# Kernel optimization log

Measured on AMD Instinct MI355X. Metric: run time of the kernel, lower is better.

## Reference

```python
import jax, jax.numpy as jnp
import numpy as np

WINDOW = 8
NUM_HEADS = 12


def setup_inputs() -> dict:
    key = jax.random.key(0)
    k1, k2, k3 = jax.random.split(key, 3)
    B, H, W, C = 32, 64, 64, 384
    x = jax.random.normal(k1, (B, H, W, C), dtype=jnp.float32)
    w_qkv = jax.random.normal(k2, (C, 3 * C), dtype=jnp.float32) * (C ** -0.5)
    w_proj = jax.random.normal(k3, (C, C), dtype=jnp.float32) * (C ** -0.5)
    b_proj = jnp.zeros((C,), dtype=jnp.float32)
    return {"x": x, "w_qkv": w_qkv, "w_proj": w_proj, "b_proj": b_proj}


def window_partition(x, ws):
    B, H, W, C = x.shape
    x = x.reshape(B, H // ws, ws, W // ws, ws, C)
    x = x.transpose(0, 1, 3, 2, 4, 5)  # [B, nH, nW, ws, ws, C]
    return x.reshape(-1, ws * ws, C)


def window_reverse(x, ws, H, W):
    nWin = (H // ws) * (W // ws)
    B = x.shape[0] // nWin
    C = x.shape[2]
    x = x.reshape(B, H // ws, W // ws, ws, ws, C)
    x = x.transpose(0, 1, 3, 2, 4, 5)
    return x.reshape(B, H, W, C)


def reference(x, w_qkv, w_proj, b_proj):
    B, H, W, C = x.shape
    ws = WINDOW
    nh = NUM_HEADS
    hd = C // nh
    scale = hd ** -0.5
    N = ws * ws

    xw = window_partition(x, ws)                      # [nW*B, N, C]
    qkv = xw @ w_qkv                                  # [nW*B, N, 3C]
    qkv = qkv.reshape(-1, N, 3, nh, hd)
    qkv = qkv.transpose(2, 0, 3, 1, 4)                # [3, nW*B, nh, N, hd]
    q, k, v = qkv[0], qkv[1], qkv[2]

    attn = jnp.einsum('whnd,whmd->whnm', q, k) * scale  # [nW*B, nh, N, N]
    attn = jax.nn.softmax(attn, axis=-1)
    out = jnp.einsum('whnm,whmd->whnd', attn, v)         # [nW*B, nh, N, hd]
    out = out.transpose(0, 2, 1, 3).reshape(-1, N, C)    # [nW*B, N, C]
    out = out @ w_proj + b_proj
    return window_reverse(out, ws, H, W)
```

## Files before the change

kernel.cpp:

```cpp
#include <hip/hip_runtime.h>


typedef __attribute__((ext_vector_type(8))) short bf16x8;
typedef __attribute__((ext_vector_type(4))) float f32x4;
typedef __attribute__((ext_vector_type(4))) short short4_t;

__device__ __forceinline__ short f2bf(float f) {
    union { float f; unsigned u; } v; v.f = f;
    unsigned r = v.u + 0x7fffu + ((v.u >> 16) & 1u);
    return (short)(r >> 16);
}

__device__ __forceinline__ unsigned pk2(float a, float b) {
    return ((unsigned)(unsigned short)f2bf(b) << 16) | (unsigned short)f2bf(a);
}

__device__ __forceinline__ f32x4 mfma16(bf16x8 a, bf16x8 b, f32x4 c) {
    return __builtin_amdgcn_mfma_f32_16x16x32_bf16(a, b, c, 0, 0, 0);
}

__device__ __forceinline__ short4_t pack4(f32x4 v) {
    short4_t s;
    s.x = f2bf(v[0]); s.y = f2bf(v[1]); s.z = f2bf(v[2]); s.w = f2bf(v[3]);
    return s;
}

__device__ __forceinline__ void gload_lds16(const void* g, void* l) {
    __builtin_amdgcn_global_load_lds(
        (const __attribute__((address_space(1))) unsigned int*)g,
        (__attribute__((address_space(3))) unsigned int*)l, 16, 0, 0);
}

__device__ __forceinline__ void drain_vmem() {
    asm volatile("s_waitcnt vmcnt(0)" ::: "memory");
    __builtin_amdgcn_sched_barrier(0);
}

__global__ void prep_weights(const float* __restrict__ wqkv, const float* __restrict__ wproj,
                             short* __restrict__ wq_fm, short* __restrict__ wp_t) {
    const int QKV_ELEMS = 12 * 96 * 384;
    int i = blockIdx.x * 256 + threadIdx.x;
    if (i < QKV_ELEMS) {
        int e    = i & 7;
        int f    = i >> 3;
        int row  = f % 48;
        int kk   = (f / 48) % 12;
        int g    = (f / (48 * 12)) % 4;
        int half = (f / (48 * 12 * 4)) & 1;
        int h    = f / (48 * 12 * 4 * 2);
        int grow = half * 48 + row;
        int k    = kk * 32 + g * 8 + e;
        int col  = (grow >> 5) * 384 + h * 32 + (grow & 31);
        float w = wqkv[k * 1152 + col];
        if (grow < 32) w *= 0.17677669529663687f;
        wq_fm[i] = f2bf(w);
    } else if (i < QKV_ELEMS + 384 * 384) {
        int j = i - QKV_ELEMS;
        int n = j / 384, k = j % 384;
        wp_t[j] = f2bf(wproj[k * 384 + n]);
    }
}

__global__ __launch_bounds__(512, 4)
void qkv_attn(const float* __restrict__ x, const short* __restrict__ wq_fm,
              short* __restrict__ y_sw) {
    __shared__ short Wl[48 * 384];
    __shared__ short k_s[2][64 * 40];
    __shared__ short v_t[2][32 * 72];
    __shared__ short ps[2][64 * 72];

    const int tid   = threadIdx.x;
    const int lane  = tid & 63;
    const int wid   = tid >> 6;
    const int col16 = lane & 15;
    const int kgrp  = lane >> 4;
    const int w     = wid >> 2;
    const int quad  = wid & 3;

    const int win = blockIdx.x * 2 + w;
    const int b = win >> 6, wi = win & 63, whr = wi >> 3, wwc = wi & 7;
    const float* xbase = x + (((b * 64) + whr * 8) * 64 + wwc * 8) * 384;

    const char* Wb = (const char*)Wl + kgrp * 9216 + col16 * 16;

    for (int i = wid; i < 36; i += 8)
        gload_lds16(wq_fm + i * 512 + lane * 8, &Wl[i * 512]);

    bf16x8 xf[12];
    {
        int t = quad * 16 + col16;
        const float* xr = xbase + ((t >> 3) * 64 + (t & 7)) * 384;
#pragma unroll
        for (int kk = 0; kk < 12; ++kk) {
            const float* p0 = xr + kk * 32 + kgrp * 8;
            float4 a = *reinterpret_cast<const float4*>(p0);
            float4 c = *reinterpret_cast<const float4*>(p0 + 4);
            bf16x8 f;
            f[0] = f2bf(a.x); f[1] = f2bf(a.y); f[2] = f2bf(a.z); f[3] = f2bf(a.w);
            f[4] = f2bf(c.x); f[5] = f2bf(c.y); f[6] = f2bf(c.z); f[7] = f2bf(c.w);
            xf[kk] = f;
        }
    }

    const int g = win * 64 + quad * 16 + col16;
    const int mtile = g >> 7, yrow = g & 127;
    char* ybase = (char*)y_sw + (size_t)mtile * 98304 + (size_t)yrow * 128;

    for (int h = 0; h < 12; ++h) {
        drain_vmem();
        __syncthreads();

        f32x4 aQ0 = (f32x4){0.f, 0.f, 0.f, 0.f};
        f32x4 aQ1 = (f32x4){0.f, 0.f, 0.f, 0.f};
        f32x4 aK0 = (f32x4){0.f, 0.f, 0.f, 0.f};
#pragma unroll
        for (int kk = 0; kk < 12; ++kk) {
            bf16x8 wf0 = *reinterpret_cast<const bf16x8*>(Wb + kk * 768);
            bf16x8 wf1 = *reinterpret_cast<const bf16x8*>(Wb + kk * 768 + 256);
            bf16x8 wf2 = *reinterpret_cast<const bf16x8*>(Wb + kk * 768 + 512);
            aQ0 = mfma16(wf0, xf[kk], aQ0);
            aQ1 = mfma16(wf1, xf[kk], aQ1);
            aK0 = mfma16(wf2, xf[kk], aK0);
        }

        __syncthreads();

        {
            const short* src = wq_fm + h * 36864 + 18432;
            for (int i = wid; i < 36; i += 8)
                gload_lds16(src + i * 512 + lane * 8, &Wl[i * 512]);
        }

        bf16x8 qa;
        {
            unsigned A0 = pk2(aQ0[0], aQ0[1]);
            unsigned A1 = pk2(aQ0[2], aQ0[3]);
            unsigned B0 = pk2(aQ1[0], aQ1[1]);
            unsigned B1 = pk2(aQ1[2], aQ1[3]);
            int s0 = ((kgrp & 1) * 2) * 16 + col16;
            int a0 = __shfl((int)A0, s0, 64),      a1 = __shfl((int)A1, s0, 64);
            int a2 = __shfl((int)A0, s0 + 16, 64), a3 = __shfl((int)A1, s0 + 16, 64);
            int b0 = __shfl((int)B0, s0, 64),      b1 = __shfl((int)B1, s0, 64);
            int b2 = __shfl((int)B0, s0 + 16, 64), b3 = __shfl((int)B1, s0 + 16, 64);
            union { int i[4]; bf16x8 v; } qu;
            const bool loHalf = (kgrp < 2);
            qu.i[0] = loHalf ? a0 : b0;
            qu.i[1] = loHalf ? a1 : b1;
            qu.i[2] = loHalf ? a2 : b2;
            qu.i[3] = loHalf ? a3 : b3;
            qa = qu.v;
        }
        *reinterpret_cast<short4_t*>(
            &k_s[w][(quad * 16 + col16) * 40 + kgrp * 4]) = pack4(aK0);

        drain_vmem();
        __syncthreads();

        f32x4 aK1 = (f32x4){0.f, 0.f, 0.f, 0.f};
        f32x4 aV0 = (f32x4){0.f, 0.f, 0.f, 0.f};
        f32x4 aV1 = (f32x4){0.f, 0.f, 0.f, 0.f};
#pragma unroll
        for (int kk = 0; kk < 12; ++kk) {
            bf16x8 wfK  = *reinterpret_cast<const bf16x8*>(Wb + kk * 768);
            bf16x8 wfV0 = *reinterpret_cast<const bf16x8*>(Wb + kk * 768 + 256);
            bf16x8 wfV1 = *reinterpret_cast<const bf16x8*>(Wb + kk * 768 + 512);
            aK1 = mfma16(wfK, xf[kk], aK1);
            aV0 = mfma16(xf[kk], wfV0, aV0);
            aV1 = mfma16(xf[kk], wfV1, aV1);
        }
        *reinterpret_cast<short4_t*>(
            &k_s[w][(quad * 16 + col16) * 40 + 16 + kgrp * 4]) = pack4(aK1);
        *reinterpret_cast<short4_t*>(
            &v_t[w][(col16) * 72 + quad * 16 + kgrp * 4]) = pack4(aV0);
        *reinterpret_cast<short4_t*>(
            &v_t[w][(16 + col16) * 72 + quad * 16 + kgrp * 4]) = pack4(aV1);

        __syncthreads();

        if (h < 11) {
            const short* src = wq_fm + (h + 1) * 36864;
            for (int i = wid; i < 36; i += 8)
                gload_lds16(src + i * 512 + lane * 8, &Wl[i * 512]);
        }

        f32x4 sc[4];
#pragma unroll
        for (int nt = 0; nt < 4; ++nt) {
            bf16x8 kf = *reinterpret_cast<const bf16x8*>(
                &k_s[w][(nt * 16 + col16) * 40 + kgrp * 8]);
            f32x4 z = (f32x4){0.f, 0.f, 0.f, 0.f};
            sc[nt] = mfma16(kf, qa, z);
        }
        float m = sc[0][0];
#pragma unroll
        for (int nt = 0; nt < 4; ++nt)
#pragma unroll
            for (int r = 0; r < 4; ++r) m = fmaxf(m, sc[nt][r]);
        m = fmaxf(m, __shfl_xor(m, 16, 64));
        m = fmaxf(m, __shfl_xor(m, 32, 64));
        float s = 0.f;
#pragma unroll
        for (int nt = 0; nt < 4; ++nt)
#pragma unroll
            for (int r = 0; r < 4; ++r) {
                sc[nt][r] = __expf(sc[nt][r] - m);
                s += sc[nt][r];
            }
        s += __shfl_xor(s, 16, 64);
        s += __shfl_xor(s, 32, 64);
        float inv = 1.0f / s;
#pragma unroll
        for (int nt = 0; nt < 4; ++nt) {
            f32x4 pv;
            pv[0] = sc[nt][0] * inv; pv[1] = sc[nt][1] * inv;
            pv[2] = sc[nt][2] * inv; pv[3] = sc[nt][3] * inv;
            *reinterpret_cast<short4_t*>(
                &ps[w][(quad * 16 + col16) * 72 + nt * 16 + kgrp * 4]) = pack4(pv);
        }
        f32x4 o2[2];
        o2[0] = (f32x4){0.f, 0.f, 0.f, 0.f};
        o2[1] = (f32x4){0.f, 0.f, 0.f, 0.f};
#pragma unroll
        for (int kt = 0; kt < 2; ++kt) {
            bf16x8 pb = *reinterpret_cast<const bf16x8*>(
                &ps[w][(quad * 16 + col16) * 72 + kt * 32 + kgrp * 8]);
#pragma unroll
            for (int d = 0; d < 2; ++d) {
                bf16x8 va = *reinterpret_cast<const bf16x8*>(
                    &v_t[w][(d * 16 + col16) * 72 + kt * 32 + kgrp * 8]);
                o2[d] = mfma16(va, pb, o2[d]);
            }
        }
#pragma unroll
        for (int d = 0; d < 2; ++d) {
            int c0 = h * 32 + d * 16 + kgrp * 4;
            int kchunk = c0 >> 6;
            int koff = (2 * (c0 & 63)) ^ ((yrow & 7) << 4);
            *reinterpret_cast<short4_t*>(ybase + kchunk * 16384 + koff) = pack4(o2[d]);
        }
    }
}

__global__ __launch_bounds__(256)
void proj_gemm(const short* __restrict__ y_sw, const short* __restrict__ wp_t,
               const float* __restrict__ b_proj, float* __restrict__ out) {
    __shared__ short At[2][128 * 64];

    const int tid = threadIdx.x, lane = tid & 63, wv = tid >> 6;
    const int col16 = lane & 15, kgrp = lane >> 4;
    const int wm = wv >> 1, wn = wv & 1;
    const int mtile = blockIdx.x;
    const int nblk  = blockIdx.y;

    const short* asrc = y_sw + (size_t)mtile * 6 * 128 * 64;

    for (int i = wv; i < 16; i += 4)
        gload_lds16(asrc + i * 512 + lane * 8, &At[0][i * 512]);

    const short* bptr[4];
#pragma unroll
    for (int nt = 0; nt < 4; ++nt)
        bptr[nt] = wp_t + (size_t)(nblk * 128 + wn * 64 + nt * 16 + col16) * 384;

    f32x4 acc[4][4];
#pragma unroll
    for (int i = 0; i < 4; ++i)
#pragma unroll
        for (int j = 0; j < 4; ++j) acc[i][j] = (f32x4){0.f, 0.f, 0.f, 0.f};

    int cur = 0;
    for (int ks = 0; ks < 6; ++ks) {
        drain_vmem();
        __syncthreads();
        if (ks < 5) {
            const short* src = asrc + (ks + 1) * (128 * 64);
            for (int i = wv; i < 16; i += 4)
                gload_lds16(src + i * 512 + lane * 8, &At[cur ^ 1][i * 512]);
        }
#pragma unroll
        for (int kk = 0; kk < 2; ++kk) {
            const int kbyte = kk * 64 + kgrp * 16;
            bf16x8 af[4];
#pragma unroll
            for (int mt = 0; mt < 4; ++mt) {
                const int r = wm * 64 + mt * 16 + col16;
                af[mt] = *reinterpret_cast<const bf16x8*>(
                    (const char*)At[cur] + r * 128 + (kbyte ^ ((r & 7) << 4)));
            }
#pragma unroll
            for (int nt = 0; nt < 4; ++nt) {
                bf16x8 bf = *reinterpret_cast<const bf16x8*>(bptr[nt] + ks * 64 + kk * 32 + kgrp * 8);
#pragma unroll
                for (int mt = 0; mt < 4; ++mt)
                    acc[mt][nt] = mfma16(af[mt], bf, acc[mt][nt]);
            }
        }
        cur ^= 1;
    }

#pragma unroll
    for (int nt = 0; nt < 4; ++nt) {
        int c = nblk * 128 + wn * 64 + nt * 16 + col16;
        float bias = b_proj[c];
#pragma unroll
        for (int mt = 0; mt < 4; ++mt) {
#pragma unroll
            for (int r = 0; r < 4; ++r) {
                int gg = mtile * 128 + wm * 64 + mt * 16 + kgrp * 4 + r;
                int win = gg >> 6, t = gg & 63;
                int b = win >> 6, whr = (win >> 3) & 7, wwc = win & 7;
                int orow = (b * 64 + whr * 8 + (t >> 3)) * 64 + wwc * 8 + (t & 7);
                out[(size_t)orow * 384 + c] = acc[mt][nt][r] + bias;
            }
        }
    }
}

__global__ __launch_bounds__(512, 2)
void win_attn_fused(const float* __restrict__ x, const short* __restrict__ wq_fm,
                    const short* __restrict__ wp_t, const float* __restrict__ b_proj,
                    float* __restrict__ out) {
    __shared__ short Wl[96 * 384];
    __shared__ short q_s[2][64 * 40];
    __shared__ short k_s[2][64 * 40];
    __shared__ short v_t[2][32 * 72];
    __shared__ short ps[2][64 * 72];

    const int tid   = threadIdx.x;
    const int lane  = tid & 63;
    const int wv    = tid >> 6;
    const int col16 = lane & 15;
    const int kgrp  = lane >> 4;
    const int wwin  = wv >> 2;
    const int q4    = wv & 3;
    const int wm    = q4 >> 1, wn = q4 & 1;

    const int win = blockIdx.x * 2 + wwin;
    const int b = win >> 6, wi = win & 63, whr = wi >> 3, wwc = wi & 7;
    const float* xbase = x + (((b * 64) + whr * 8) * 64 + wwc * 8) * 384;

    const char* Wb = (const char*)Wl + kgrp * 9216 + col16 * 16;

    for (int i = 0; i < 9; ++i) {
        int chunk = wv * 9 + i;
        gload_lds16(wq_fm + chunk * 512 + lane * 8, &Wl[chunk * 512]);
    }
    bf16x8 xf[12];
    {
        int t = q4 * 16 + col16;
        const float* xr = xbase + ((t >> 3) * 64 + (t & 7)) * 384;
#pragma unroll
        for (int kk = 0; kk < 12; ++kk) {
            const float* p0 = xr + kk * 32 + kgrp * 8;
            float4 a = *reinterpret_cast<const float4*>(p0);
            float4 c = *reinterpret_cast<const float4*>(p0 + 4);
            bf16x8 f;
            f[0] = f2bf(a.x); f[1] = f2bf(a.y); f[2] = f2bf(a.z); f[3] = f2bf(a.w);
            f[4] = f2bf(c.x); f[5] = f2bf(c.y); f[6] = f2bf(c.z); f[7] = f2bf(c.w);
            xf[kk] = f;
        }
    }
    f32x4 pacc[2][12];
#pragma unroll
    for (int i = 0; i < 2; ++i)
#pragma unroll
        for (int j = 0; j < 12; ++j) pacc[i][j] = (f32x4){0.f, 0.f, 0.f, 0.f};

    for (int h = 0; h < 12; ++h) {
        drain_vmem();
        __syncthreads();
        f32x4 acc[6];
#pragma unroll
        for (int i = 0; i < 6; ++i) acc[i] = (f32x4){0.f, 0.f, 0.f, 0.f};
#pragma unroll
        for (int kk = 0; kk < 12; ++kk) {
#pragma unroll
            for (int rd = 0; rd < 6; ++rd) {
                const bf16x8 wf = *reinterpret_cast<const bf16x8*>(
                    Wb + (rd / 3) * 36864 + kk * 768 + (rd % 3) * 256);
                if (rd < 4) acc[rd] = mfma16(wf, xf[kk], acc[rd]);
                else        acc[rd] = mfma16(xf[kk], wf, acc[rd]);
            }
        }
#pragma unroll
        for (int rd = 0; rd < 4; ++rd) {
            short* dst = (rd < 2) ? q_s[wwin] : k_s[wwin];
            *reinterpret_cast<short4_t*>(
                &dst[(q4 * 16 + col16) * 40 + (rd & 1) * 16 + kgrp * 4]) = pack4(acc[rd]);
        }
#pragma unroll
        for (int d = 0; d < 2; ++d)
            *reinterpret_cast<short4_t*>(
                &v_t[wwin][(d * 16 + col16) * 72 + q4 * 16 + kgrp * 4]) = pack4(acc[4 + d]);

        __syncthreads();
        if (h < 11) {
            const short* src = wq_fm + (h + 1) * 36864;
            for (int i = 0; i < 9; ++i) {
                int chunk = wv * 9 + i;
                gload_lds16(src + chunk * 512 + lane * 8, &Wl[chunk * 512]);
            }
        }
        bf16x8 qa = *reinterpret_cast<const bf16x8*>(
            &q_s[wwin][(q4 * 16 + col16) * 40 + kgrp * 8]);
        f32x4 sc[4];
#pragma unroll
        for (int nt = 0; nt < 4; ++nt) {
            bf16x8 kf = *reinterpret_cast<const bf16x8*>(
                &k_s[wwin][(nt * 16 + col16) * 40 + kgrp * 8]);
            f32x4 z = (f32x4){0.f, 0.f, 0.f, 0.f};
            sc[nt] = mfma16(qa, kf, z);
        }
        float mx[4], sm[4], p[4][4];
#pragma unroll
        for (int r = 0; r < 4; ++r)
            mx[r] = fmaxf(fmaxf(sc[0][r], sc[1][r]), fmaxf(sc[2][r], sc[3][r]));
#pragma unroll
        for (int d = 1; d < 16; d <<= 1)
#pragma unroll
            for (int r = 0; r < 4; ++r) mx[r] = fmaxf(mx[r], __shfl_xor(mx[r], d, 16));
#pragma unroll
        for (int r = 0; r < 4; ++r) {
            sm[r] = 0.f;
#pragma unroll
            for (int nt = 0; nt < 4; ++nt) { p[nt][r] = __expf(sc[nt][r] - mx[r]); sm[r] += p[nt][r]; }
        }
#pragma unroll
        for (int d = 1; d < 16; d <<= 1)
#pragma unroll
            for (int r = 0; r < 4; ++r) sm[r] += __shfl_xor(sm[r], d, 16);
#pragma unroll
        for (int r = 0; r < 4; ++r) {
            float inv = 1.0f / sm[r];
            int prow = q4 * 16 + kgrp * 4 + r;
#pragma unroll
            for (int nt = 0; nt < 4; ++nt)
                ps[wwin][prow * 72 + nt * 16 + col16] = f2bf(p[nt][r] * inv);
        }
        f32x4 o2[2];
        o2[0] = (f32x4){0.f, 0.f, 0.f, 0.f};
        o2[1] = (f32x4){0.f, 0.f, 0.f, 0.f};
#pragma unroll
        for (int kt = 0; kt < 2; ++kt) {
            bf16x8 pb = *reinterpret_cast<const bf16x8*>(
                &ps[wwin][(q4 * 16 + col16) * 72 + kt * 32 + kgrp * 8]);
#pragma unroll
            for (int d = 0; d < 2; ++d) {
                bf16x8 va = *reinterpret_cast<const bf16x8*>(
                    &v_t[wwin][(d * 16 + col16) * 72 + kt * 32 + kgrp * 8]);
                o2[d] = mfma16(va, pb, o2[d]);
            }
        }
#pragma unroll
        for (int d = 0; d < 2; ++d)
            *reinterpret_cast<short4_t*>(
                &ps[wwin][(q4 * 16 + col16) * 72 + d * 16 + kgrp * 4]) = pack4(o2[d]);
        __syncthreads();
#pragma unroll
        for (int mt = 0; mt < 2; ++mt) {
            bf16x8 ya = *reinterpret_cast<const bf16x8*>(
                &ps[wwin][(wm * 32 + mt * 16 + col16) * 72 + kgrp * 8]);
#pragma unroll
            for (int nt = 0; nt < 12; ++nt) {
                bf16x8 wb = *reinterpret_cast<const bf16x8*>(
                    &wp_t[(wn * 192 + nt * 16 + col16) * 384 + h * 32 + kgrp * 8]);
                pacc[mt][nt] = mfma16(ya, wb, pacc[mt][nt]);
            }
        }
    }
#pragma unroll
    for (int nt = 0; nt < 12; ++nt) {
        int c = wn * 192 + nt * 16 + col16;
        float bias = b_proj[c];
#pragma unroll
        for (int mt = 0; mt < 2; ++mt) {
#pragma unroll
            for (int r = 0; r < 4; ++r) {
                int token = wm * 32 + mt * 16 + kgrp * 4 + r;
                int hh = whr * 8 + (token >> 3);
                int ww2 = wwc * 8 + (token & 7);
                out[(((b * 64) + hh) * 64 + ww2) * 384 + c] = pacc[mt][nt][r] + bias;
            }
        }
    }
}

extern "C" void kernel_launch(void* const* d_in, const int* in_sizes, int n_in,
                              void* d_out, int out_size, void* d_ws, size_t ws_size,
                              hipStream_t stream) {
    const float* x     = (const float*)d_in[0];
    const float* wqkv  = (const float*)d_in[1];
    const float* wproj = (const float*)d_in[2];
    const float* bproj = (const float*)d_in[3];

    short* wq_fm = (short*)d_ws;
    short* wp_t  = wq_fm + 12 * 96 * 384;
    short* y_sw  = wp_t + 384 * 384;
    const size_t need = (size_t)(12 * 96 * 384 + 384 * 384) * 2 + (size_t)1024 * 6 * 128 * 128;

    prep_weights<<<2304, 256, 0, stream>>>(wqkv, wproj, wq_fm, wp_t);
    if (ws_size >= need) {
        qkv_attn<<<1024, 512, 0, stream>>>(x, wq_fm, y_sw);
        proj_gemm<<<dim3(1024, 3), 256, 0, stream>>>(y_sw, wp_t, bproj, (float*)d_out);
    } else {
        win_attn_fused<<<1024, 512, 0, stream>>>(x, wq_fm, wp_t, bproj, (float*)d_out);
    }
}
```

Baseline: 317.6 us.

## Split QKV projection across wave halves with double-width weight tile per head

Loads the full per-head Q/K/V weight slice (96 rows) into LDS at once, removing the mid-head reload and one barrier pair. Each wave now handles 32 tokens of one window, with half the waves computing Q and the first K half and the other half computing the second K half and V, so each weight fragment feeds two MFMAs. The softmax is done only by the Q waves, which adds an extra barrier before the PV product and leaves half the waves idle during scores. LDS use roughly doubles and launch bounds drop to 2 blocks per CU, so occupancy is lower.

```diff
diff --git a/kernel.cpp b/kernel.cpp
--- a/kernel.cpp
+++ b/kernel.cpp
@@ -61,10 +61,10 @@
     }
 }
 
-__global__ __launch_bounds__(512, 4)
+__global__ __launch_bounds__(512, 2)
 void qkv_attn(const float* __restrict__ x, const short* __restrict__ wq_fm,
               short* __restrict__ y_sw) {
-    __shared__ short Wl[48 * 384];
+    __shared__ short Wl[96 * 384];
     __shared__ short k_s[2][64 * 40];
     __shared__ short v_t[2][32 * 72];
     __shared__ short ps[2][64 * 72];
@@ -74,21 +74,24 @@
     const int wid   = tid >> 6;
     const int col16 = lane & 15;
     const int kgrp  = lane >> 4;
-    const int w     = wid >> 2;
-    const int quad  = wid & 3;
+    const int dh    = wid >> 2;
+    const int w     = (wid >> 1) & 1;
+    const int th    = wid & 1;
+    const int quad  = dh * 2 + th;
 
     const int win = blockIdx.x * 2 + w;
     const int b = win >> 6, wi = win & 63, whr = wi >> 3, wwc = wi & 7;
     const float* xbase = x + (((b * 64) + whr * 8) * 64 + wwc * 8) * 384;
 
-    const char* Wb = (const char*)Wl + kgrp * 9216 + col16 * 16;
-
-    for (int i = wid; i < 36; i += 8)
+    const char* Wb = (const char*)Wl + dh * 36864 + kgrp * 9216 + col16 * 16;
+
+    for (int i = wid; i < 72; i += 8)
         gload_lds16(wq_fm + i * 512 + lane * 8, &Wl[i * 512]);
 
-    bf16x8 xf[12];
-    {
-        int t = quad * 16 + col16;
+    bf16x8 xf[2][12];
+#pragma unroll
+    for (int nt = 0; nt < 2; ++nt) {
+        int t = th * 32 + nt * 16 + col16;
         const float* xr = xbase + ((t >> 3) * 64 + (t & 7)) * 384;
 #pragma unroll
         for (int kk = 0; kk < 12; ++kk) {
@@ -98,7 +101,7 @@
             bf16x8 f;
             f[0] = f2bf(a.x); f[1] = f2bf(a.y); f[2] = f2bf(a.z); f[3] = f2bf(a.w);
             f[4] = f2bf(c.x); f[5] = f2bf(c.y); f[6] = f2bf(c.z); f[7] = f2bf(c.w);
-            xf[kk] = f;
+            xf[nt][kk] = f;
         }
     }
 
@@ -110,113 +113,133 @@
         drain_vmem();
         __syncthreads();
 
-        f32x4 aQ0 = (f32x4){0.f, 0.f, 0.f, 0.f};
-        f32x4 aQ1 = (f32x4){0.f, 0.f, 0.f, 0.f};
-        f32x4 aK0 = (f32x4){0.f, 0.f, 0.f, 0.f};
-#pragma unroll
-        for (int kk = 0; kk < 12; ++kk) {
-            bf16x8 wf0 = *reinterpret_cast<const bf16x8*>(Wb + kk * 768);
-            bf16x8 wf1 = *reinterpret_cast<const bf16x8*>(Wb + kk * 768 + 256);
-            bf16x8 wf2 = *reinterpret_cast<const bf16x8*>(Wb + kk * 768 + 512);
-            aQ0 = mfma16(wf0, xf[kk], aQ0);
-            aQ1 = mfma16(wf1, xf[kk], aQ1);
-            aK0 = mfma16(wf2, xf[kk], aK0);
-        }
-
-        __syncthreads();
-
-        {
-            const short* src = wq_fm + h * 36864 + 18432;
-            for (int i = wid; i < 36; i += 8)
-                gload_lds16(src + i * 512 + lane * 8, &Wl[i * 512]);
-        }
-
-        bf16x8 qa;
-        {
-            unsigned A0 = pk2(aQ0[0], aQ0[1]);
-            unsigned A1 = pk2(aQ0[2], aQ0[3]);
-            unsigned B0 = pk2(aQ1[0], aQ1[1]);
-            unsigned B1 = pk2(aQ1[2], aQ1[3]);
-            int s0 = ((kgrp & 1) * 2) * 16 + col16;
-            int a0 = __shfl((int)A0, s0, 64),      a1 = __shfl((int)A1, s0, 64);
-            int a2 = __shfl((int)A0, s0 + 16, 64), a3 = __shfl((int)A1, s0 + 16, 64);
-            int b0 = __shfl((int)B0, s0, 64),      b1 = __shfl((int)B1, s0, 64);
-            int b2 = __shfl((int)B0, s0 + 16, 64), b3 = __shfl((int)B1, s0 + 16, 64);
-            union { int i[4]; bf16x8 v; } qu;
-            const bool loHalf = (kgrp < 2);
-            qu.i[0] = loHalf ? a0 : b0;
-            qu.i[1] = loHalf ? a1 : b1;
-            qu.i[2] = loHalf ? a2 : b2;
-            qu.i[3] = loHalf ? a3 : b3;
-            qa = qu.v;
-        }
-        *reinterpret_cast<short4_t*>(
-            &k_s[w][(quad * 16 + col16) * 40 + kgrp * 4]) = pack4(aK0);
-
-        drain_vmem();
-        __syncthreads();
-
-        f32x4 aK1 = (f32x4){0.f, 0.f, 0.f, 0.f};
-        f32x4 aV0 = (f32x4){0.f, 0.f, 0.f, 0.f};
-        f32x4 aV1 = (f32x4){0.f, 0.f, 0.f, 0.f};
-#pragma unroll
-        for (int kk = 0; kk < 12; ++kk) {
-            bf16x8 wfK  = *reinterpret_cast<const bf16x8*>(Wb + kk * 768);
-            bf16x8 wfV0 = *reinterpret_cast<const bf16x8*>(Wb + kk * 768 + 256);
-            bf16x8 wfV1 = *reinterpret_cast<const bf16x8*>(Wb + kk * 768 + 512);
-            aK1 = mfma16(wfK, xf[kk], aK1);
-            aV0 = mfma16(xf[kk], wfV0, aV0);
-            aV1 = mfma16(xf[kk], wfV1, aV1);
-        }
-        *reinterpret_cast<short4_t*>(
-            &k_s[w][(quad * 16 + col16) * 40 + 16 + kgrp * 4]) = pack4(aK1);
-        *reinterpret_cast<short4_t*>(
-            &v_t[w][(col16) * 72 + quad * 16 + kgrp * 4]) = pack4(aV0);
-        *reinterpret_cast<short4_t*>(
-            &v_t[w][(16 + col16) * 72 + quad * 16 + kgrp * 4]) = pack4(aV1);
+        f32x4 acc[3][2];
+#pragma unroll
+        for (int i = 0; i < 3; ++i)
+#pragma unroll
+            for (int j = 0; j < 2; ++j) acc[i][j] = (f32x4){0.f, 0.f, 0.f, 0.f};
+
+        if (dh == 0) {
+#pragma unroll
+            for (int kk = 0; kk < 12; ++kk) {
+                bf16x8 wf0 = *reinterpret_cast<const bf16x8*>(Wb + kk * 768);
+                bf16x8 wf1 = *reinterpret_cast<const bf16x8*>(Wb + kk * 768 + 256);
+                bf16x8 wf2 = *reinterpret_cast<const bf16x8*>(Wb + kk * 768 + 512);
+#pragma unroll
+                for (int nt = 0; nt < 2; ++nt) {
+                    acc[0][nt] = mfma16(wf0, xf[nt][kk], acc[0][nt]);
+                    acc[1][nt] = mfma16(wf1, xf[nt][kk], acc[1][nt]);
+                    acc[2][nt] = mfma16(wf2, xf[nt][kk], acc[2][nt]);
+                }
+            }
+        } else {
+#pragma unroll
+            for (int kk = 0; kk < 12; ++kk) {
+                bf16x8 wfK  = *reinterpret_cast<const bf16x8*>(Wb + kk * 768);
+                bf16x8 wfV0 = *reinterpret_cast<const bf16x8*>(Wb + kk * 768 + 256);
+                bf16x8 wfV1 = *reinterpret_cast<const bf16x8*>(Wb + kk * 768 + 512);
+#pragma unroll
+                for (int nt = 0; nt < 2; ++nt) {
+                    acc[0][nt] = mfma16(wfK, xf[nt][kk], acc[0][nt]);
+                    acc[1][nt] = mfma16(xf[nt][kk], wfV0, acc[1][nt]);
+                    acc[2][nt] = mfma16(xf[nt][kk], wfV1, acc[2][nt]);
+                }
+            }
+        }
+
+        bf16x8 qa[2];
+        if (dh == 0) {
+#pragma unroll
+            for (int nt = 0; nt < 2; ++nt) {
+                unsigned A0 = pk2(acc[0][nt][0], acc[0][nt][1]);
+                unsigned A1 = pk2(acc[0][nt][2], acc[0][nt][3]);
+                unsigned B0 = pk2(acc[1][nt][0], acc[1][nt][1]);
+                unsigned B1 = pk2(acc[1][nt][2], acc[1][nt][3]);
+                int s0 = ((kgrp & 1) * 2) * 16 + col16;
+                int a0 = __shfl((int)A0, s0, 64),      a1 = __shfl((int)A1, s0, 64);
+                int a2 = __shfl((int)A0, s0 + 16, 64), a3 = __shfl((int)A1, s0 + 16, 64);
+                int b0 = __shfl((int)B0, s0, 64),      b1 = __shfl((int)B1, s0, 64);
+                int b2 = __shfl((int)B0, s0 + 16, 64), b3 = __shfl((int)B1, s0 + 16, 64);
+                union { int i[4]; bf16x8 v; } qu;
+                const bool loHalf = (kgrp < 2);
+                qu.i[0] = loHalf ? a0 : b0;
+                qu.i[1] = loHalf ? a1 : b1;
+                qu.i[2] = loHalf ? a2 : b2;
+                qu.i[3] = loHalf ? a3 : b3;
+                qa[nt] = qu.v;
+            }
+#pragma unroll
+            for (int nt = 0; nt < 2; ++nt)
+                *reinterpret_cast<short4_t*>(
+                    &k_s[w][(th * 32 + nt * 16 + col16) * 40 + kgrp * 4]) = pack4(acc[2][nt]);
+        } else {
+#pragma unroll
+            for (int nt = 0; nt < 2; ++nt)
+                *reinterpret_cast<short4_t*>(
+                    &k_s[w][(th * 32 + nt * 16 + col16) * 40 + 16 + kgrp * 4]) = pack4(acc[0][nt]);
+#pragma unroll
+            for (int vt = 0; vt < 2; ++vt)
+#pragma unroll
+                for (int nt = 0; nt < 2; ++nt)
+                    *reinterpret_cast<short4_t*>(
+                        &v_t[w][(vt * 16 + col16) * 72 + th * 32 + nt * 16 + kgrp * 4]) =
+                        pack4(acc[1 + vt][nt]);
+        }
 
         __syncthreads();
 
         if (h < 11) {
             const short* src = wq_fm + (h + 1) * 36864;
-            for (int i = wid; i < 36; i += 8)
+            for (int i = wid; i < 72; i += 8)
                 gload_lds16(src + i * 512 + lane * 8, &Wl[i * 512]);
         }
 
-        f32x4 sc[4];
-#pragma unroll
-        for (int nt = 0; nt < 4; ++nt) {
-            bf16x8 kf = *reinterpret_cast<const bf16x8*>(
-                &k_s[w][(nt * 16 + col16) * 40 + kgrp * 8]);
-            f32x4 z = (f32x4){0.f, 0.f, 0.f, 0.f};
-            sc[nt] = mfma16(kf, qa, z);
-        }
-        float m = sc[0][0];
-#pragma unroll
-        for (int nt = 0; nt < 4; ++nt)
-#pragma unroll
-            for (int r = 0; r < 4; ++r) m = fmaxf(m, sc[nt][r]);
-        m = fmaxf(m, __shfl_xor(m, 16, 64));
-        m = fmaxf(m, __shfl_xor(m, 32, 64));
-        float s = 0.f;
-#pragma unroll
-        for (int nt = 0; nt < 4; ++nt)
-#pragma unroll
-            for (int r = 0; r < 4; ++r) {
-                sc[nt][r] = __expf(sc[nt][r] - m);
-                s += sc[nt][r];
-            }
-        s += __shfl_xor(s, 16, 64);
-        s += __shfl_xor(s, 32, 64);
-        float inv = 1.0f / s;
-#pragma unroll
-        for (int nt = 0; nt < 4; ++nt) {
-            f32x4 pv;
-            pv[0] = sc[nt][0] * inv; pv[1] = sc[nt][1] * inv;
-            pv[2] = sc[nt][2] * inv; pv[3] = sc[nt][3] * inv;
-            *reinterpret_cast<short4_t*>(
-                &ps[w][(quad * 16 + col16) * 72 + nt * 16 + kgrp * 4]) = pack4(pv);
-        }
+        if (dh == 0) {
+            bf16x8 kf[4];
+#pragma unroll
+            for (int kt = 0; kt < 4; ++kt)
+                kf[kt] = *reinterpret_cast<const bf16x8*>(
+                    &k_s[w][(kt * 16 + col16) * 40 + kgrp * 8]);
+#pragma unroll
+            for (int nt = 0; nt < 2; ++nt) {
+                f32x4 sc[4];
+#pragma unroll
+                for (int kt = 0; kt < 4; ++kt) {
+                    f32x4 z = (f32x4){0.f, 0.f, 0.f, 0.f};
+                    sc[kt] = mfma16(kf[kt], qa[nt], z);
+                }
+                float m = sc[0][0];
+#pragma unroll
+                for (int kt = 0; kt < 4; ++kt)
+#pragma unroll
+                    for (int r = 0; r < 4; ++r) m = fmaxf(m, sc[kt][r]);
+                m = fmaxf(m, __shfl_xor(m, 16, 64));
+                m = fmaxf(m, __shfl_xor(m, 32, 64));
+                float s = 0.f;
+#pragma unroll
+                for (int kt = 0; kt < 4; ++kt)
+#pragma unroll
+                    for (int r = 0; r < 4; ++r) {
+                        sc[kt][r] = __expf(sc[kt][r] - m);
+                        s += sc[kt][r];
+                    }
+                s += __shfl_xor(s, 16, 64);
+                s += __shfl_xor(s, 32, 64);
+                float inv = 1.0f / s;
+                int prow = th * 32 + nt * 16 + col16;
+#pragma unroll
+                for (int kt = 0; kt < 4; ++kt) {
+                    f32x4 pv;
+                    pv[0] = sc[kt][0] * inv; pv[1] = sc[kt][1] * inv;
+                    pv[2] = sc[kt][2] * inv; pv[3] = sc[kt][3] * inv;
+                    *reinterpret_cast<short4_t*>(
+                        &ps[w][prow * 72 + kt * 16 + kgrp * 4]) = pack4(pv);
+                }
+            }
+        }
+
+        __syncthreads();
+
         f32x4 o2[2];
         o2[0] = (f32x4){0.f, 0.f, 0.f, 0.f};
         o2[1] = (f32x4){0.f, 0.f, 0.f, 0.f};
```

After: 361.7 us. +13.9%, slower.
